# Kernel optimization log

Measured on AMD Instinct MI355X. Metric: run time of the kernel, lower is better.

The kernel has to match this reference:

```python
import jax, jax.numpy as jnp
import numpy as np

H = 8   # num_heads
D = 64  # out_features per head

def setup_inputs() -> dict:
    key = jax.random.key(0)
    k1, k2, k3, k4 = jax.random.split(key, 4)
    B, N, F_IN, E = 2, 8192, 512, 65536
    x = jax.random.normal(k1, (B, N, F_IN), dtype=jnp.float32)
    edge_indices = jax.random.randint(k2, (2, E), 0, N)
    W = jax.random.normal(k3, (H * D, F_IN), dtype=jnp.float32) * (1.0 / np.sqrt(F_IN))
    a = jax.random.normal(k4, (2 * D, 1), dtype=jnp.float32) * 0.1
    return {"x": x, "edge_indices": edge_indices, "W": W, "a": a}

def reference(x, edge_indices, W, a):
    # Faithful translation of GraphAttentionLayer.forward (eval mode: dropout = identity).
    B, N, _ = x.shape
    h = (x @ W.T).reshape(B, N, H, D)              # [B,N,H,D]
    src, dst = edge_indices[0], edge_indices[1]
    E = src.shape[0]
    h_src = h[:, src]                               # [B,E,H,D]
    h_dst = h[:, dst]                               # [B,E,H,D]
    # cat([h_src,h_dst]) @ a  ==  h_src @ a[:D] + h_dst @ a[D:]
    a1, a2 = a[:D, 0], a[D:, 0]
    scores = jnp.einsum('behd,d->beh', h_src, a1) + jnp.einsum('behd,d->beh', h_dst, a2)
    scores = jax.nn.leaky_relu(scores, negative_slope=0.2)      # [B,E,H]
    # NOTE: original code softmaxes over the BATCH dim (dim=0) per edge.
    sm = jax.nn.softmax(scores, axis=0)                          # [B,E,H]
    last_edge = jnp.full((N,), -1, dtype=jnp.int32).at[src].max(
        jnp.arange(E, dtype=jnp.int32))                          # [N]
    has_edge = last_edge >= 0
    w = jnp.where(has_edge[None, :, None],
                  sm[:, jnp.clip(last_edge, 0)], 0.0)            # [B,N,H]
    # aggregated[:, s] += w[:, s, :, None] * h_dst[:, e] for each edge e with src[e]==s
    # (weights fully built before aggregation loop) => w[s] * segment_sum(h_dst over src)
    agg_dst = jnp.zeros((B, N, H, D), dtype=h.dtype).at[:, src].add(h_dst)
    aggregated = w[..., None] * agg_dst                          # [B,N,H,D]
    return aggregated.mean(axis=2)                               # [B,N,D]
```

## Files before the change

### kernel.cpp

```cpp
#include <hip/hip_runtime.h>
#include <stdint.h>

#define H_HEADS 8
#define DDIM 64
#define NNODES 8192
#define BB 2
#define FIN 512
#define FOUT 512
#define EDGES 65536
#define CAP 32

typedef unsigned short u16;
typedef unsigned int u32;
typedef __bf16 bf16x8 __attribute__((ext_vector_type(8)));
typedef float f32x4 __attribute__((ext_vector_type(4)));

__device__ __forceinline__ u16 f2bf(float f) {
    u32 u = __float_as_uint(f);
    return (u16)((u + 0x7FFFu + ((u >> 16) & 1u)) >> 16);
}
__device__ __forceinline__ float bf2f(u32 s) {
    return __uint_as_float(s << 16);
}

#define NXB (BB * NNODES * FIN / 8 / 256)
#define NWB (FOUT * FIN / 8 / 256)
#define NEB 64
__global__ __launch_bounds__(256) void prep_kernel(
    const float* __restrict__ x, const float* __restrict__ W,
    const int* __restrict__ src, const int* __restrict__ dst,
    u16* __restrict__ xb, u16* __restrict__ Wb, int* __restrict__ cursor,
    int* __restrict__ last_edge, int* __restrict__ csr_dst) {
    int blk = blockIdx.x;
    if (blk < NXB + NWB) {
        const float* in = (blk < NXB) ? x : W;
        u16* out = (blk < NXB) ? xb : Wb;
        int i = (blk < NXB ? blk : blk - NXB) * 256 + threadIdx.x;
        const float4* p = (const float4*)in;
        float4 v0 = p[(size_t)i * 2], v1 = p[(size_t)i * 2 + 1];
        u32 w0 = f2bf(v0.x) | ((u32)f2bf(v0.y) << 16);
        u32 w1 = f2bf(v0.z) | ((u32)f2bf(v0.w) << 16);
        u32 w2 = f2bf(v1.x) | ((u32)f2bf(v1.y) << 16);
        u32 w3 = f2bf(v1.z) | ((u32)f2bf(v1.w) << 16);
        ((uint4*)out)[i] = make_uint4(w0, w1, w2, w3);
    } else {
        int t = (blk - NXB - NWB) * 256 + threadIdx.x;
#pragma unroll
        for (int k = 0; k < 4; k++) {
            int e = t * 4 + k;
            int s = src[e], d = dst[e];
            int slot = atomicAdd(&cursor[s], 1);
            if (slot < CAP) csr_dst[(size_t)s * CAP + slot] = d;
            atomicMax(&last_edge[s], e);
        }
    }
}

#define GLDS(g, l)                                                              \
    __builtin_amdgcn_global_load_lds(                                           \
        (const __attribute__((address_space(1))) u32*)(g),                      \
        (__attribute__((address_space(3))) u32*)(l), 16, 0, 0)

__global__ __launch_bounds__(256) void gemm_mfma(const u16* __restrict__ A,
                                                 const u16* __restrict__ Bm,
                                                 const float* __restrict__ a,
                                                 u16* __restrict__ C,
                                                 float* __restrict__ s1,
                                                 float* __restrict__ s2) {
    __shared__ u16 As[128 * 32];
    __shared__ u16 Bs[128 * 32];
    int tid = threadIdx.x;
    int m0 = blockIdx.y * 128, n0 = blockIdx.x * 128;
    int lane = tid & 63, wv = tid >> 6;
    int wr = (wv >> 1) * 64, wc = (wv & 1) * 64;
    int l15 = lane & 15, quad = lane >> 4;
    f32x4 acc[4][4] = {};

    float a1v[4], a2v[4];
#pragma unroll
    for (int j = 0; j < 4; j++) {
        a1v[j] = a[j * 16 + l15];
        a2v[j] = a[DDIM + j * 16 + l15];
    }

    int srow = tid >> 2;
    int scol = (tid & 3) * 8;
    const u16* Ag = A + (size_t)(m0 + srow) * FIN + scol;
    const u16* Bg = Bm + (size_t)(n0 + srow) * FIN + scol;
    u16* Al = As + tid * 8;
    u16* Bl = Bs + tid * 8;

    for (int k0 = 0; k0 < FIN; k0 += 32) {
        __syncthreads();
        GLDS(Ag + k0, Al);
        GLDS(Ag + k0 + (size_t)64 * FIN, Al + 64 * 32);
        GLDS(Bg + k0, Bl);
        GLDS(Bg + k0 + (size_t)64 * FIN, Bl + 64 * 32);
        __syncthreads();
        bf16x8 af[4], bfr[4];
#pragma unroll
        for (int i = 0; i < 4; i++)
            af[i] = *(const bf16x8*)(As + (wr + i * 16 + l15) * 32 + quad * 8);
#pragma unroll
        for (int j = 0; j < 4; j++)
            bfr[j] = *(const bf16x8*)(Bs + (wc + j * 16 + l15) * 32 + quad * 8);
#pragma unroll
        for (int i = 0; i < 4; i++)
#pragma unroll
            for (int j = 0; j < 4; j++)
                acc[i][j] = __builtin_amdgcn_mfma_f32_16x16x32_bf16(
                    af[i], bfr[j], acc[i][j], 0, 0, 0);
    }

#pragma unroll
    for (int i = 0; i < 4; i++) {
        int row_base = m0 + wr + i * 16 + quad * 4;
#pragma unroll
        for (int j = 0; j < 4; j++) {
            int col = n0 + wc + j * 16 + l15;
#pragma unroll
            for (int r = 0; r < 4; r++)
                C[(size_t)(row_base + r) * FOUT + col] = f2bf(acc[i][j][r]);
        }
    }

    int head = blockIdx.x * 2 + (wv & 1);
#pragma unroll
    for (int i = 0; i < 4; i++) {
#pragma unroll
        for (int r = 0; r < 4; r++) {
            float p1 = 0.f, p2 = 0.f;
#pragma unroll
            for (int j = 0; j < 4; j++) {
                p1 += a1v[j] * acc[i][j][r];
                p2 += a2v[j] * acc[i][j][r];
            }
#pragma unroll
            for (int m = 1; m <= 8; m <<= 1) {
                p1 += __shfl_xor(p1, m);
                p2 += __shfl_xor(p2, m);
            }
            if (l15 == 0) {
                int row = m0 + wr + i * 16 + quad * 4 + r;
                s1[row * H_HEADS + head] = p1;
                s2[row * H_HEADS + head] = p2;
            }
        }
    }
}

__global__ __launch_bounds__(256) void aggregate(const u16* __restrict__ h,
                                                 const float* __restrict__ s1,
                                                 const float* __restrict__ s2,
                                                 const int* __restrict__ cursor,
                                                 const int* __restrict__ last_edge,
                                                 const int* __restrict__ dst,
                                                 const int* __restrict__ csr_dst,
                                                 float* __restrict__ out, int N) {
    int n = blockIdx.x * 2 + (threadIdx.x >> 7);
    int b = (threadIdx.x >> 6) & 1;
    int lane = threadIdx.x & 63;
    int head = lane >> 3;

    int deg = cursor[n];
    deg = deg < CAP ? deg : CAP;

    float wgt = 0.f;
    if (deg > 0) {
        int dl = dst[last_edge[n]];
        float sc0 = s1[(0 * N + n) * H_HEADS + head] +
                    s2[((size_t)0 * N + dl) * H_HEADS + head];
        float sc1 = s1[((size_t)1 * N + n) * H_HEADS + head] +
                    s2[((size_t)1 * N + dl) * H_HEADS + head];
        sc0 = sc0 >= 0.f ? sc0 : 0.2f * sc0;
        sc1 = sc1 >= 0.f ? sc1 : 0.2f * sc1;
        float m = fmaxf(sc0, sc1);
        float e0 = __expf(sc0 - m), e1 = __expf(sc1 - m);
        wgt = (b == 0 ? e0 : e1) / (e0 + e1);
    }

    float acc[8] = {};
    const u16* hb = h + (size_t)b * N * FOUT + lane * 8;
    const int* cp = csr_dst + (size_t)n * CAP;
    int dn = (deg > 0) ? cp[0] : 0;
    for (int j = 0; j < deg; j++) {
        int dn_next = (j + 1 < deg) ? cp[j + 1] : 0;
        uint4 v = *(const uint4*)(hb + (size_t)dn * FOUT);
        acc[0] += bf2f(v.x & 0xffffu);
        acc[1] += bf2f(v.x >> 16);
        acc[2] += bf2f(v.y & 0xffffu);
        acc[3] += bf2f(v.y >> 16);
        acc[4] += bf2f(v.z & 0xffffu);
        acc[5] += bf2f(v.z >> 16);
        acc[6] += bf2f(v.w & 0xffffu);
        acc[7] += bf2f(v.w >> 16);
        dn = dn_next;
    }
    float val[8];
#pragma unroll
    for (int k = 0; k < 8; k++) val[k] = acc[k] * wgt;
#pragma unroll
    for (int m = 8; m <= 32; m <<= 1)
#pragma unroll
        for (int k = 0; k < 8; k++) val[k] += __shfl_xor(val[k], m);
    if (lane < 8) {
        float* op = out + ((size_t)b * N + n) * DDIM + lane * 8;
        const float inv = 1.0f / H_HEADS;
        *(float4*)op = make_float4(val[0] * inv, val[1] * inv, val[2] * inv,
                                   val[3] * inv);
        *(float4*)(op + 4) = make_float4(val[4] * inv, val[5] * inv,
                                         val[6] * inv, val[7] * inv);
    }
}

extern "C" void kernel_launch(void* const* d_in, const int* in_sizes, int n_in,
                              void* d_out, int out_size, void* d_ws,
                              size_t ws_size, hipStream_t stream) {
    const float* x = (const float*)d_in[0];
    const int* edges = (const int*)d_in[1];
    const float* W = (const float*)d_in[2];
    const float* a = (const float*)d_in[3];
    float* out = (float*)d_out;

    const int* src = edges;
    const int* dst = edges + EDGES;

    char* p = (char*)d_ws;
    auto carve = [&](size_t bytes) {
        char* r = p;
        p += (bytes + 255) & ~(size_t)255;
        return r;
    };
    u16* xb = (u16*)carve((size_t)BB * NNODES * FIN * 2);
    u16* Wb = (u16*)carve((size_t)FOUT * FIN * 2);
    u16* h = (u16*)carve((size_t)BB * NNODES * FOUT * 2);
    float* s1 = (float*)carve((size_t)BB * NNODES * H_HEADS * 4);
    float* s2 = (float*)carve((size_t)BB * NNODES * H_HEADS * 4);
    int* cursor = (int*)carve(NNODES * 4);
    int* last_edge = (int*)carve(NNODES * 4);
    int* csr_dst = (int*)carve((size_t)NNODES * CAP * 4);

    const int M = BB * NNODES;

    hipMemsetAsync(cursor, 0, 2 * NNODES * 4, stream);
    prep_kernel<<<NXB + NWB + NEB, 256, 0, stream>>>(x, W, src, dst, xb, Wb,
                                                     cursor, last_edge, csr_dst);
    gemm_mfma<<<dim3(FOUT / 128, M / 128), 256, 0, stream>>>(xb, Wb, a, h, s1,
                                                             s2);
    aggregate<<<NNODES / 2, 256, 0, stream>>>(h, s1, s2, cursor, last_edge, dst,
                                              csr_dst, out, NNODES);
}
```

Before: 138.3 us.

## Fuse x fp32-to-bf16 conversion into GEMM tile loads; batch CSR index loads

Drops the separate pass that converts x to bf16 in the prep kernel. The GEMM now reads fp32 x directly, converts it in registers and stores bf16 into LDS, which saves writing and re-reading a 16 MB intermediate. Because the GEMM grid has four column blocks, each x tile is now read in fp32 four times through regular loads rather than async LDS loads, which may raise GEMM load latency. The aggregate kernel also loads all CSR neighbour indices once per wave, broadcasts them with shuffles and unrolls the gather loop by four so several loads are in flight.

```diff
diff --git a/kernel.cpp b/kernel.cpp
--- a/kernel.cpp
+++ b/kernel.cpp
@@ -22,29 +22,28 @@
 __device__ __forceinline__ float bf2f(u32 s) {
     return __uint_as_float(s << 16);
 }
-
-#define NXB (BB * NNODES * FIN / 8 / 256)
+__device__ __forceinline__ uint4 pack8(float4 a, float4 b) {
+    return make_uint4(f2bf(a.x) | ((u32)f2bf(a.y) << 16),
+                      f2bf(a.z) | ((u32)f2bf(a.w) << 16),
+                      f2bf(b.x) | ((u32)f2bf(b.y) << 16),
+                      f2bf(b.z) | ((u32)f2bf(b.w) << 16));
+}
+
 #define NWB (FOUT * FIN / 8 / 256)
 #define NEB 64
 __global__ __launch_bounds__(256) void prep_kernel(
-    const float* __restrict__ x, const float* __restrict__ W,
-    const int* __restrict__ src, const int* __restrict__ dst,
-    u16* __restrict__ xb, u16* __restrict__ Wb, int* __restrict__ cursor,
-    int* __restrict__ last_edge, int* __restrict__ csr_dst) {
+    const float* __restrict__ W, const int* __restrict__ src,
+    const int* __restrict__ dst, u16* __restrict__ Wb,
+    int* __restrict__ cursor, int* __restrict__ last_edge,
+    int* __restrict__ csr_dst) {
     int blk = blockIdx.x;
-    if (blk < NXB + NWB) {
-        const float* in = (blk < NXB) ? x : W;
-        u16* out = (blk < NXB) ? xb : Wb;
-        int i = (blk < NXB ? blk : blk - NXB) * 256 + threadIdx.x;
-        const float4* p = (const float4*)in;
+    if (blk < NWB) {
+        int i = blk * 256 + threadIdx.x;
+        const float4* p = (const float4*)W;
         float4 v0 = p[(size_t)i * 2], v1 = p[(size_t)i * 2 + 1];
-        u32 w0 = f2bf(v0.x) | ((u32)f2bf(v0.y) << 16);
-        u32 w1 = f2bf(v0.z) | ((u32)f2bf(v0.w) << 16);
-        u32 w2 = f2bf(v1.x) | ((u32)f2bf(v1.y) << 16);
-        u32 w3 = f2bf(v1.z) | ((u32)f2bf(v1.w) << 16);
-        ((uint4*)out)[i] = make_uint4(w0, w1, w2, w3);
+        ((uint4*)Wb)[i] = pack8(v0, v1);
     } else {
-        int t = (blk - NXB - NWB) * 256 + threadIdx.x;
+        int t = (blk - NWB) * 256 + threadIdx.x;
 #pragma unroll
         for (int k = 0; k < 4; k++) {
             int e = t * 4 + k;
@@ -61,7 +60,7 @@
         (const __attribute__((address_space(1))) u32*)(g),                      \
         (__attribute__((address_space(3))) u32*)(l), 16, 0, 0)
 
-__global__ __launch_bounds__(256) void gemm_mfma(const u16* __restrict__ A,
+__global__ __launch_bounds__(256) void gemm_mfma(const float* __restrict__ X,
                                                  const u16* __restrict__ Bm,
                                                  const float* __restrict__ a,
                                                  u16* __restrict__ C,
@@ -85,17 +84,21 @@
 
     int srow = tid >> 2;
     int scol = (tid & 3) * 8;
-    const u16* Ag = A + (size_t)(m0 + srow) * FIN + scol;
+    const float* Ag = X + (size_t)(m0 + srow) * FIN + scol;
     const u16* Bg = Bm + (size_t)(n0 + srow) * FIN + scol;
     u16* Al = As + tid * 8;
     u16* Bl = Bs + tid * 8;
 
     for (int k0 = 0; k0 < FIN; k0 += 32) {
         __syncthreads();
-        GLDS(Ag + k0, Al);
-        GLDS(Ag + k0 + (size_t)64 * FIN, Al + 64 * 32);
         GLDS(Bg + k0, Bl);
         GLDS(Bg + k0 + (size_t)64 * FIN, Bl + 64 * 32);
+        float4 fa0 = *(const float4*)(Ag + k0);
+        float4 fa1 = *(const float4*)(Ag + k0 + 4);
+        float4 fb0 = *(const float4*)(Ag + k0 + (size_t)64 * FIN);
+        float4 fb1 = *(const float4*)(Ag + k0 + (size_t)64 * FIN + 4);
+        *(uint4*)Al = pack8(fa0, fa1);
+        *(uint4*)(Al + 64 * 32) = pack8(fb0, fb1);
         __syncthreads();
         bf16x8 af[4], bfr[4];
 #pragma unroll
@@ -179,22 +182,27 @@
         wgt = (b == 0 ? e0 : e1) / (e0 + e1);
     }
 
+    const int* cp = csr_dst + (size_t)n * CAP;
+    int myidx = (lane < CAP) ? cp[lane] : 0;
+
     float acc[8] = {};
     const u16* hb = h + (size_t)b * N * FOUT + lane * 8;
-    const int* cp = csr_dst + (size_t)n * CAP;
-    int dn = (deg > 0) ? cp[0] : 0;
-    for (int j = 0; j < deg; j++) {
-        int dn_next = (j + 1 < deg) ? cp[j + 1] : 0;
-        uint4 v = *(const uint4*)(hb + (size_t)dn * FOUT);
-        acc[0] += bf2f(v.x & 0xffffu);
-        acc[1] += bf2f(v.x >> 16);
-        acc[2] += bf2f(v.y & 0xffffu);
-        acc[3] += bf2f(v.y >> 16);
-        acc[4] += bf2f(v.z & 0xffffu);
-        acc[5] += bf2f(v.z >> 16);
-        acc[6] += bf2f(v.w & 0xffffu);
-        acc[7] += bf2f(v.w >> 16);
-        dn = dn_next;
+    for (int j0 = 0; j0 < deg; j0 += 4) {
+#pragma unroll
+        for (int k = 0; k < 4; k++) {
+            int j = j0 + k;
+            float f = (j < deg) ? 1.0f : 0.0f;
+            int dn = (j < deg) ? __shfl(myidx, j) : 0;
+            uint4 v = *(const uint4*)(hb + (size_t)dn * FOUT);
+            acc[0] = fmaf(f, bf2f(v.x & 0xffffu), acc[0]);
+            acc[1] = fmaf(f, bf2f(v.x >> 16), acc[1]);
+            acc[2] = fmaf(f, bf2f(v.y & 0xffffu), acc[2]);
+            acc[3] = fmaf(f, bf2f(v.y >> 16), acc[3]);
+            acc[4] = fmaf(f, bf2f(v.z & 0xffffu), acc[4]);
+            acc[5] = fmaf(f, bf2f(v.z >> 16), acc[5]);
+            acc[6] = fmaf(f, bf2f(v.w & 0xffffu), acc[6]);
+            acc[7] = fmaf(f, bf2f(v.w >> 16), acc[7]);
+        }
     }
     float val[8];
 #pragma unroll
@@ -231,7 +239,6 @@
         p += (bytes + 255) & ~(size_t)255;
         return r;
     };
-    u16* xb = (u16*)carve((size_t)BB * NNODES * FIN * 2);
     u16* Wb = (u16*)carve((size_t)FOUT * FIN * 2);
     u16* h = (u16*)carve((size_t)BB * NNODES * FOUT * 2);
     float* s1 = (float*)carve((size_t)BB * NNODES * H_HEADS * 4);
@@ -243,9 +250,9 @@
     const int M = BB * NNODES;
 
     hipMemsetAsync(cursor, 0, 2 * NNODES * 4, stream);
-    prep_kernel<<<NXB + NWB + NEB, 256, 0, stream>>>(x, W, src, dst, xb, Wb,
-                                                     cursor, last_edge, csr_dst);
-    gemm_mfma<<<dim3(FOUT / 128, M / 128), 256, 0, stream>>>(xb, Wb, a, h, s1,
+    prep_kernel<<<NWB + NEB, 256, 0, stream>>>(W, src, dst, Wb, cursor,
+                                               last_edge, csr_dst);
+    gemm_mfma<<<dim3(FOUT / 128, M / 128), 256, 0, stream>>>(x, Wb, a, h, s1,
                                                              s2);
     aggregate<<<NNODES / 2, 256, 0, stream>>>(h, s1, s2, cursor, last_edge, dst,
                                               csr_dst, out, NNODES);
```

Result: faster. 131.1 us (-5.2%).
